# Kernel optimization log

Measured on AMD Instinct MI355X. Metric: run time of the kernel, lower is better.

## Reference

```python
import jax, jax.numpy as jnp
import numpy as np

N = 4096          # nodes (single graph, batch=None)
E = 65536         # edges (avg degree 16)
C = 256           # hidden_channels
L = 3             # num_layers
H = 8             # attention heads
EPS = 1e-5        # batchnorm eps


def setup_inputs() -> dict:
    key = jax.random.key(0)
    ks = iter(jax.random.split(key, 64))
    s = 0.05
    d = {}
    d['x'] = jax.random.normal(next(ks), (N, 1), dtype=jnp.float32)
    d['edge_index'] = jax.random.randint(next(ks), (2, E), 0, N, dtype=jnp.int32)
    # input projection Linear(1, C)
    d['lin1_w'] = jax.random.normal(next(ks), (C, 1), dtype=jnp.float32) * s
    d['lin1_b'] = jnp.zeros((C,), dtype=jnp.float32)
    # GIN MLP: Linear(C,C) -> ReLU -> Linear(C,C), stacked over layers
    d['gin_w1'] = jax.random.normal(next(ks), (L, C, C), dtype=jnp.float32) * s
    d['gin_b1'] = jnp.zeros((L, C), dtype=jnp.float32)
    d['gin_w2'] = jax.random.normal(next(ks), (L, C, C), dtype=jnp.float32) * s
    d['gin_b2'] = jnp.zeros((L, C), dtype=jnp.float32)
    # MultiheadAttention projections
    for nm in ['attn_wq', 'attn_wk', 'attn_wv', 'attn_wo']:
        d[nm] = jax.random.normal(next(ks), (L, C, C), dtype=jnp.float32) * s
    for nm in ['attn_bq', 'attn_bk', 'attn_bv', 'attn_bo']:
        d[nm] = jnp.zeros((L, C), dtype=jnp.float32)
    # three BatchNorms per GPSConv layer
    for nm in ['bn1', 'bn2', 'bn3']:
        d[nm + '_g'] = jnp.ones((L, C), dtype=jnp.float32)
        d[nm + '_b'] = jnp.zeros((L, C), dtype=jnp.float32)
    # GPSConv feedforward: Linear(C, 2C) -> ReLU -> Linear(2C, C)
    d['mlp_w1'] = jax.random.normal(next(ks), (L, 2 * C, C), dtype=jnp.float32) * s
    d['mlp_b1'] = jnp.zeros((L, 2 * C), dtype=jnp.float32)
    d['mlp_w2'] = jax.random.normal(next(ks), (L, C, 2 * C), dtype=jnp.float32) * s
    d['mlp_b2'] = jnp.zeros((L, C), dtype=jnp.float32)
    return d


def _bn(v, g, b):
    # training-mode BatchNorm1d over the node dimension (biased variance)
    m = v.mean(0)
    var = v.var(0)
    return (v - m) * jax.lax.rsqrt(var + EPS) * g + b


def _gps_forward(x, edge_index, lin1_w, lin1_b, gin_w1, gin_b1, gin_w2, gin_b2,
                 attn_wq, attn_bq, attn_wk, attn_bk, attn_wv, attn_bv,
                 attn_wo, attn_bo, bn1_g, bn1_b, bn2_g, bn2_b, bn3_g, bn3_b,
                 mlp_w1, mlp_b1, mlp_w2, mlp_b2):
    h = x @ lin1_w.T + lin1_b                     # [N, C]
    src, dst = edge_index[0], edge_index[1]
    dh = C // H
    scale = 1.0 / jnp.sqrt(jnp.float32(dh))
    for l in range(L):
        xin = h
        # --- GIN branch: gather -> scatter-sum -> MLP ---
        agg = jax.ops.segment_sum(xin[src], dst, num_segments=N)   # [N, C]
        z = xin + agg                                               # eps=0
        z = jax.nn.relu(z @ gin_w1[l].T + gin_b1[l]) @ gin_w2[l].T + gin_b2[l]
        h1 = _bn(z + xin, bn1_g[l], bn1_b[l])
        # --- global multihead attention over all N nodes ---
        q = (xin @ attn_wq[l].T + attn_bq[l]).reshape(N, H, dh)
        k = (xin @ attn_wk[l].T + attn_bk[l]).reshape(N, H, dh)
        v = (xin @ attn_wv[l].T + attn_bv[l]).reshape(N, H, dh)
        scores = jnp.einsum('nhd,mhd->hnm', q, k) * scale           # [H, N, N]
        a = jax.nn.softmax(scores, axis=-1)
        o = jnp.einsum('hnm,mhd->nhd', a, v).reshape(N, C)
        o = o @ attn_wo[l].T + attn_bo[l]
        h2 = _bn(o + xin, bn2_g[l], bn2_b[l])
        # --- combine + feedforward ---
        s = h1 + h2
        m = jax.nn.relu(s @ mlp_w1[l].T + mlp_b1[l]) @ mlp_w2[l].T + mlp_b2[l]
        h = _bn(s + m, bn3_g[l], bn3_b[l])
    return h


def reference(x, edge_index, lin1_w, lin1_b, gin_w1, gin_b1, gin_w2, gin_b2,
              attn_wq, attn_bq, attn_wk, attn_bk, attn_wv, attn_bv,
              attn_wo, attn_bo, bn1_g, bn1_b, bn2_g, bn2_b, bn3_g, bn3_b,
              mlp_w1, mlp_b1, mlp_w2, mlp_b2):
    return _gps_forward(x, edge_index, lin1_w, lin1_b, gin_w1, gin_b1, gin_w2,
                        gin_b2, attn_wq, attn_bq, attn_wk, attn_bk, attn_wv,
                        attn_bv, attn_wo, attn_bo, bn1_g, bn1_b, bn2_g, bn2_b,
                        bn3_g, bn3_b, mlp_w1, mlp_b1, mlp_w2, mlp_b2)
```

## Files before the change

kernel.cpp:

```cpp
#include <hip/hip_runtime.h>

#define NN 4096
#define NE 65536
#define C 256
#define NL 3
#define NH 8
#define DH 32
#define EPS 1e-5f
#define SPLIT 2
#define KT8 (NN/128/SPLIT)
#define SR 512

typedef __bf16 bf16x8 __attribute__((ext_vector_type(8)));
typedef __bf16 bf16x4v __attribute__((ext_vector_type(4)));
typedef float f32x4 __attribute__((ext_vector_type(4)));
typedef short bf16x4s __attribute__((ext_vector_type(4)));

#define QSCALE (0.17677669529663687f * 1.4426950408889634f)

#define CC1 (C*C)
#define GS 72

__global__ __launch_bounds__(256) void prep_w(const float* __restrict__ s0,
        const float* __restrict__ s1, const float* __restrict__ s2,
        const float* __restrict__ s3, const float* __restrict__ s4,
        const float* __restrict__ s5, const float* __restrict__ s6,
        const float* __restrict__ s7, __bf16* __restrict__ dst) {
    int g = blockIdx.y;
    int i = (blockIdx.x*256 + threadIdx.x)*4;
    const float* src; int n;
    switch (g) {
        case 0: src=s0; n=3*CC1; break;
        case 1: src=s1; n=3*CC1; break;
        case 2: src=s2; n=3*CC1; break;
        case 3: src=s3; n=3*CC1; break;
        case 4: src=s4; n=3*CC1; break;
        case 5: src=s5; n=3*CC1; break;
        case 6: src=s6; n=6*CC1; break;
        default: src=s7; n=6*CC1; break;
    }
    if (i >= n) return;
    size_t off;
    if (g >= 2 && g <= 4) {
        int l = i >> 16, rem = i & (CC1-1);
        off = (size_t)(6 + 3*l + (g-2))*CC1 + rem;
    } else {
        size_t base = (g==0) ? 0 : (g==1) ? 3*(size_t)CC1 : (g==5) ? 15*(size_t)CC1
                    : (g==6) ? 18*(size_t)CC1 : 24*(size_t)CC1;
        off = base + i;
    }
    float4 t = *(const float4*)(src + i);
    bf16x4v o = {(__bf16)t.x, (__bf16)t.y, (__bf16)t.z, (__bf16)t.w};
    *(bf16x4v*)(dst + off) = o;
}

__global__ __launch_bounds__(256) void lin1_kernel(const float* __restrict__ x,
        const float* __restrict__ w, const float* __restrict__ b,
        __bf16* __restrict__ out) {
    int n = blockIdx.x, c = threadIdx.x;
    out[(size_t)n*C + c] = (__bf16)(x[n]*w[c] + b[c]);
}

__global__ __launch_bounds__(256) void hist_kernel(const int* __restrict__ ei,
        int* __restrict__ cnt) {
    int e = blockIdx.x*256 + threadIdx.x;
    atomicAdd(&cnt[ei[NE + e]], 1);
}

__global__ __launch_bounds__(256) void scan_kernel(const int* __restrict__ cnt,
        int* __restrict__ rowptr, int* __restrict__ cursor) {
    __shared__ int tot[256];
    __shared__ int pre[257];
    int t = threadIdx.x;
    int base = t*16;
    int local[16];
    int s = 0;
    #pragma unroll
    for (int i = 0; i < 16; i++) { local[i] = s; s += cnt[base+i]; }
    tot[t] = s;
    __syncthreads();
    if (t == 0) {
        int acc = 0;
        for (int i = 0; i < 256; i++) { pre[i] = acc; acc += tot[i]; }
        pre[256] = acc;
    }
    __syncthreads();
    int off = pre[t];
    #pragma unroll
    for (int i = 0; i < 16; i++) {
        rowptr[base+i] = off + local[i];
        cursor[base+i] = off + local[i];
    }
    if (t == 0) rowptr[NN] = pre[256];
}

__global__ __launch_bounds__(256) void fill_kernel(const int* __restrict__ ei,
        int* __restrict__ cursor, int* __restrict__ eidsrc) {
    int e = blockIdx.x*256 + threadIdx.x;
    int dst = ei[NE + e], src = ei[e];
    int pos = atomicAdd(&cursor[dst], 1);
    eidsrc[pos] = src;
}

template<int QKV, int BN, int COMB>
__device__ __forceinline__ void gemm_core(int bm, int bn,
        const __bf16* A, const float* A2f, const __bf16* A2b, const __bf16* W,
        const float* b0, const float* b1, const float* b2,
        const __bf16* add1, const __bf16* add2,
        __bf16* out, __bf16* vt, float* stats,
        const float* coefs,
        const float* st1, const float* g1, const float* bb1,
        const float* st2, const float* g2, const float* bb2,
        const float* lsum,
        int K, int Nout, int relu, __bf16* As, __bf16* Ws) {
    int tid = threadIdx.x;
    int wave = tid >> 6, lane = tid & 63;
    int ln = lane & 15, quad = lane >> 4;
    int row = tid >> 2, kseg = (tid & 3) * 16;
    f32x4 acc[4] = {};
    for (int k0 = 0; k0 < K; k0 += 64) {
        __syncthreads();
        {
            bf16x8 a0, a1;
            if constexpr (COMB) {
                int rowg = bm + row;
                int head = (k0 + kseg) >> 5;
                float w[SPLIT];
                float tot = 0.f;
                #pragma unroll
                for (int zz = 0; zz < SPLIT; zz++) {
                    w[zz] = lsum[((size_t)zz*NH + head)*NN + rowg];
                    tot += w[zz];
                }
                float inv = 1.0f / tot;
                float v[16] = {};
                #pragma unroll
                for (int zz = 0; zz < SPLIT; zz++) {
                    const __bf16* p = &A[((size_t)zz*NN + rowg)*C + k0 + kseg];
                    bf16x8 x0 = *(const bf16x8*)p, x1 = *(const bf16x8*)(p + 8);
                    #pragma unroll
                    for (int j = 0; j < 8; j++) {
                        v[j]   += w[zz]*(float)x0[j];
                        v[8+j] += w[zz]*(float)x1[j];
                    }
                }
                #pragma unroll
                for (int j = 0; j < 8; j++) {
                    a0[j] = (__bf16)(v[j]*inv);
                    a1[j] = (__bf16)(v[8+j]*inv);
                }
            } else {
                const __bf16* ap = &A[(size_t)(bm+row)*K + k0 + kseg];
                a0 = *(const bf16x8*)ap;
                a1 = *(const bf16x8*)(ap + 8);
                if constexpr (BN == 1) {
                    const __bf16* p = &A2b[(size_t)(bm+row)*K + k0 + kseg];
                    bf16x8 z0 = *(const bf16x8*)p;
                    bf16x8 z1v = *(const bf16x8*)(p + 8);
                    float sc1[16], sh1[16], sc2[16], sh2[16];
                    #pragma unroll
                    for (int i = 0; i < 4; i++) {
                        *(float4*)&sc1[i*4] = *(const float4*)&coefs[k0 + kseg + i*4];
                        *(float4*)&sh1[i*4] = *(const float4*)&coefs[C + k0 + kseg + i*4];
                        *(float4*)&sc2[i*4] = *(const float4*)&coefs[2*C + k0 + kseg + i*4];
                        *(float4*)&sh2[i*4] = *(const float4*)&coefs[3*C + k0 + kseg + i*4];
                    }
                    #pragma unroll
                    for (int j = 0; j < 8; j++) {
                        a0[j] = (__bf16)((float)a0[j]*sc1[j] + sh1[j]
                                       + (float)z0[j]*sc2[j] + sh2[j]);
                        a1[j] = (__bf16)((float)a1[j]*sc1[8+j] + sh1[8+j]
                                       + (float)z1v[j]*sc2[8+j] + sh2[8+j]);
                    }
                } else if (A2f) {
                    const float* p = &A2f[(size_t)(bm+row)*K + k0 + kseg];
                    float4 t0 = *(const float4*)p;
                    float4 t1 = *(const float4*)(p+4);
                    float4 t2 = *(const float4*)(p+8);
                    float4 t3 = *(const float4*)(p+12);
                    a0[0]=(__bf16)((float)a0[0]+t0.x); a0[1]=(__bf16)((float)a0[1]+t0.y);
                    a0[2]=(__bf16)((float)a0[2]+t0.z); a0[3]=(__bf16)((float)a0[3]+t0.w);
                    a0[4]=(__bf16)((float)a0[4]+t1.x); a0[5]=(__bf16)((float)a0[5]+t1.y);
                    a0[6]=(__bf16)((float)a0[6]+t1.z); a0[7]=(__bf16)((float)a0[7]+t1.w);
                    a1[0]=(__bf16)((float)a1[0]+t2.x); a1[1]=(__bf16)((float)a1[1]+t2.y);
                    a1[2]=(__bf16)((float)a1[2]+t2.z); a1[3]=(__bf16)((float)a1[3]+t2.w);
                    a1[4]=(__bf16)((float)a1[4]+t3.x); a1[5]=(__bf16)((float)a1[5]+t3.y);
                    a1[6]=(__bf16)((float)a1[6]+t3.z); a1[7]=(__bf16)((float)a1[7]+t3.w);
                }
            }
            *(bf16x8*)&As[row*GS + kseg]     = a0;
            *(bf16x8*)&As[row*GS + kseg + 8] = a1;
            const __bf16* wp = &W[(size_t)(bn+row)*K + k0 + kseg];
            *(bf16x8*)&Ws[row*GS + kseg]     = *(const bf16x8*)wp;
            *(bf16x8*)&Ws[row*GS + kseg + 8] = *(const bf16x8*)(wp + 8);
        }
        __syncthreads();
        #pragma unroll
        for (int kt2 = 0; kt2 < 2; kt2++) {
            bf16x8 bfr = *(const bf16x8*)&Ws[(wave*16+ln)*GS + kt2*32 + quad*8];
            #pragma unroll
            for (int i = 0; i < 4; i++) {
                bf16x8 afr = *(const bf16x8*)&As[(i*16+ln)*GS + kt2*32 + quad*8];
                acc[i] = __builtin_amdgcn_mfma_f32_16x16x32_bf16(afr, bfr, acc[i], 0, 0, 0);
            }
        }
    }
    int col = bn + wave*16 + ln;
    if constexpr (QKV) {
        float bsv = col < 256 ? b0[col] : (col < 512 ? b1[col-256] : b2[col-512]);
        if (col < 512) {
            float osc = col < 256 ? (float)QSCALE : 1.0f;
            #pragma unroll
            for (int i = 0; i < 4; i++)
                #pragma unroll
                for (int rr = 0; rr < 4; rr++)
                    out[(size_t)(bm + i*16 + quad*4 + rr)*SR + col] =
                        (__bf16)((acc[i][rr] + bsv) * osc);
        } else {
            int vrow = col - 512;
            #pragma unroll
            for (int i = 0; i < 4; i++) {
                bf16x4v pk = {(__bf16)(acc[i][0]+bsv), (__bf16)(acc[i][1]+bsv),
                              (__bf16)(acc[i][2]+bsv), (__bf16)(acc[i][3]+bsv)};
                *(bf16x4v*)&vt[(size_t)vrow*NN + bm + i*16 + quad*4] = pk;
            }
        }
        return;
    }
    float bsv = b0[col];
    float sc1 = 0.f, sh1 = 0.f, sc2 = 0.f, sh2 = 0.f;
    if constexpr (BN == 2) {
        float m1 = st1[col]*(1.f/NN);
        sc1 = rsqrtf(st1[C+col]*(1.f/NN) - m1*m1 + EPS) * g1[col];
        sh1 = bb1[col] - m1*sc1;
        float m2 = st2[col]*(1.f/NN);
        sc2 = rsqrtf(st2[C+col]*(1.f/NN) - m2*m2 + EPS) * g2[col];
        sh2 = bb2[col] - m2*sc2;
    }
    float ssum = 0.f, ssq = 0.f;
    #pragma unroll
    for (int i = 0; i < 4; i++) {
        #pragma unroll
        for (int rr = 0; rr < 4; rr++) {
            int rw = bm + i*16 + quad*4 + rr;
            float vv = acc[i][rr] + bsv;
            if (relu) vv = fmaxf(vv, 0.f);
            size_t idx = (size_t)rw*Nout + col;
            if constexpr (BN == 2) {
                vv += (float)add1[idx]*sc1 + sh1 + (float)add2[idx]*sc2 + sh2;
            } else {
                if (add1) vv += (float)add1[idx];
                if (add2) vv += (float)add2[idx];
            }
            out[idx] = (__bf16)vv;
            ssum += vv; ssq += vv*vv;
        }
    }
    if (stats) {
        ssum += __shfl_xor(ssum, 16); ssum += __shfl_xor(ssum, 32);
        ssq  += __shfl_xor(ssq, 16);  ssq  += __shfl_xor(ssq, 32);
        if (quad == 0) {
            atomicAdd(&stats[col], ssum);
            atomicAdd(&stats[Nout + col], ssq);
        }
    }
}

__device__ __forceinline__ void attn_body(int t, const __bf16* __restrict__ qk,
        const __bf16* __restrict__ vt, __bf16* __restrict__ opart,
        float* __restrict__ lsum, __bf16* lds) {
    int z = t >> 8, head = (t >> 5) & 7, qb = (t & 31) * 128;
    int hb = head * DH;
    int tid = threadIdx.x;
    int wave = tid >> 6, lane = tid & 63;
    int ln = lane & 15, quad = lane >> 4;
    __bf16* Kb0 = lds;
    __bf16* Kb1 = lds + 4608;

    bf16x8 qf[2];
    #pragma unroll
    for (int g = 0; g < 2; g++)
        qf[g] = *(const bf16x8*)&qk[(size_t)(qb + wave*32 + g*16 + ln)*SR + hb + quad*8];

    f32x4 ot[2][2] = {};
    float l_[2] = {0.f, 0.f};

    int srow = tid >> 1, sseg = (tid & 1) * 16;
    int kt0 = z * KT8;
    {
        const __bf16* kp = &qk[(size_t)(kt0*128 + srow)*SR + 256 + hb + sseg];
        *(bf16x8*)&Kb0[srow*36 + sseg]     = *(const bf16x8*)kp;
        *(bf16x8*)&Kb0[srow*36 + sseg + 8] = *(const bf16x8*)(kp + 8);
    }
    const __bf16* vbase = &vt[(size_t)(hb + ln)*NN + quad*4];
    const size_t vh = (size_t)16*NN;
    for (int i = 0; i < KT8; i++) {
        int kb = (kt0 + i) * 128;
        __bf16* Kc = (i & 1) ? Kb1 : Kb0;
        __bf16* Kn = (i & 1) ? Kb0 : Kb1;
        __syncthreads();
        bf16x8 nk0, nk1;
        bool hasNext = (i + 1 < KT8);
        if (hasNext) {
            const __bf16* kp = &qk[(size_t)(kb + 128 + srow)*SR + 256 + hb + sseg];
            nk0 = *(const bf16x8*)kp;
            nk1 = *(const bf16x8*)(kp + 8);
        }
        bf16x4s vfc[2][2], vfn[2][2];
        #pragma unroll
        for (int s = 0; s < 2; s++)
            #pragma unroll
            for (int h = 0; h < 2; h++)
                vfc[s][h] = *(const bf16x4s*)&vbase[vh*h + kb + s*16];
        #pragma unroll
        for (int pr = 0; pr < 4; pr++) {
            if (pr < 3) {
                #pragma unroll
                for (int s = 0; s < 2; s++)
                    #pragma unroll
                    for (int h = 0; h < 2; h++)
                        vfn[s][h] = *(const bf16x4s*)&vbase[vh*h + kb + (pr*2+2+s)*16];
            }
            bf16x8 kf0 = *(const bf16x8*)&Kc[((pr*2+0)*16+ln)*36 + quad*8];
            bf16x8 kf1 = *(const bf16x8*)&Kc[((pr*2+1)*16+ln)*36 + quad*8];
            f32x4 zz = {0.f,0.f,0.f,0.f};
            f32x4 st00 = __builtin_amdgcn_mfma_f32_16x16x32_bf16(kf0, qf[0], zz, 0, 0, 0);
            f32x4 st10 = __builtin_amdgcn_mfma_f32_16x16x32_bf16(kf0, qf[1], zz, 0, 0, 0);
            f32x4 st01 = __builtin_amdgcn_mfma_f32_16x16x32_bf16(kf1, qf[0], zz, 0, 0, 0);
            f32x4 st11 = __builtin_amdgcn_mfma_f32_16x16x32_bf16(kf1, qf[1], zz, 0, 0, 0);
            union { __bf16 b[4]; bf16x4s s; } pf00, pf01, pf10, pf11;
            #pragma unroll
            for (int rr = 0; rr < 4; rr++) {
                float p;
                p = __builtin_amdgcn_exp2f(st00[rr]); pf00.b[rr] = (__bf16)p; l_[0] += p;
                p = __builtin_amdgcn_exp2f(st01[rr]); pf01.b[rr] = (__bf16)p; l_[0] += p;
                p = __builtin_amdgcn_exp2f(st10[rr]); pf10.b[rr] = (__bf16)p; l_[1] += p;
                p = __builtin_amdgcn_exp2f(st11[rr]); pf11.b[rr] = (__bf16)p; l_[1] += p;
            }
            ot[0][0] = __builtin_amdgcn_mfma_f32_16x16x16bf16_1k(vfc[0][0], pf00.s, ot[0][0], 0, 0, 0);
            ot[0][1] = __builtin_amdgcn_mfma_f32_16x16x16bf16_1k(vfc[0][1], pf00.s, ot[0][1], 0, 0, 0);
            ot[1][0] = __builtin_amdgcn_mfma_f32_16x16x16bf16_1k(vfc[0][0], pf10.s, ot[1][0], 0, 0, 0);
            ot[1][1] = __builtin_amdgcn_mfma_f32_16x16x16bf16_1k(vfc[0][1], pf10.s, ot[1][1], 0, 0, 0);
            ot[0][0] = __builtin_amdgcn_mfma_f32_16x16x16bf16_1k(vfc[1][0], pf01.s, ot[0][0], 0, 0, 0);
            ot[0][1] = __builtin_amdgcn_mfma_f32_16x16x16bf16_1k(vfc[1][1], pf01.s, ot[0][1], 0, 0, 0);
            ot[1][0] = __builtin_amdgcn_mfma_f32_16x16x16bf16_1k(vfc[1][0], pf11.s, ot[1][0], 0, 0, 0);
            ot[1][1] = __builtin_amdgcn_mfma_f32_16x16x16bf16_1k(vfc[1][1], pf11.s, ot[1][1], 0, 0, 0);
            #pragma unroll
            for (int s = 0; s < 2; s++)
                #pragma unroll
                for (int h = 0; h < 2; h++)
                    vfc[s][h] = vfn[s][h];
        }
        if (hasNext) {
            *(bf16x8*)&Kn[srow*36 + sseg]     = nk0;
            *(bf16x8*)&Kn[srow*36 + sseg + 8] = nk1;
        }
    }
    #pragma unroll
    for (int g = 0; g < 2; g++) {
        l_[g] += __shfl_xor(l_[g], 16);
        l_[g] += __shfl_xor(l_[g], 32);
        float inv = 1.0f / l_[g];
        int qrow = qb + wave*32 + g*16 + ln;
        #pragma unroll
        for (int h = 0; h < 2; h++) {
            bf16x4v pk = {(__bf16)(ot[g][h][0]*inv), (__bf16)(ot[g][h][1]*inv),
                          (__bf16)(ot[g][h][2]*inv), (__bf16)(ot[g][h][3]*inv)};
            *(bf16x4v*)&opart[((size_t)z*NN + qrow)*C + hb + h*16 + quad*4] = pk;
        }
        if (quad == 0)
            lsum[((size_t)z*NH + head)*NN + qrow] = l_[g];
    }
}

__global__ __launch_bounds__(256) void qkv_agg_kernel(const __bf16* __restrict__ Hb,
        const __bf16* __restrict__ Wqkv, const float* __restrict__ bq,
        const float* __restrict__ bk, const float* __restrict__ bv,
        __bf16* __restrict__ qkout, __bf16* __restrict__ vtout,
        const int* __restrict__ rowptr, const int* __restrict__ eidsrc,
        float* __restrict__ agg) {
    __shared__ __bf16 lds[9216];
    int bx = blockIdx.x;
    if (bx < 768) {
        gemm_core<1,0,0>((bx & 63)*64, (bx >> 6)*64, Hb, nullptr, nullptr, Wqkv,
                bq, bk, bv, nullptr, nullptr, qkout, vtout, nullptr,
                nullptr, nullptr, nullptr, nullptr, nullptr, nullptr, nullptr,
                nullptr, C, 768, 0, lds, lds + 4608);
        return;
    }
    int tid = threadIdx.x;
    int wave = tid >> 6, lane = tid & 63;
    int node = (bx - 768)*4 + wave;
    int beg = rowptr[node], end = rowptr[node+1];
    float s0 = 0.f, s1 = 0.f, s2 = 0.f, s3 = 0.f;
    for (int e = beg; e < end; e++) {
        int src = eidsrc[e];
        bf16x4v hv = *(const bf16x4v*)&Hb[(size_t)src*C + lane*4];
        s0 += (float)hv[0]; s1 += (float)hv[1];
        s2 += (float)hv[2]; s3 += (float)hv[3];
    }
    float4 o = {s0, s1, s2, s3};
    *(float4*)&agg[(size_t)node*C + lane*4] = o;
}

__global__ __launch_bounds__(256) void gin1_attn_kernel(const __bf16* __restrict__ Hb,
        const float* __restrict__ agg, const __bf16* __restrict__ gw1,
        const float* __restrict__ gb1, __bf16* __restrict__ t1,
        const __bf16* __restrict__ qk, const __bf16* __restrict__ vt,
        __bf16* __restrict__ opart, float* __restrict__ lsum) {
    __shared__ __bf16 lds[9216];
    int bx = blockIdx.x;
    if (bx < 32*NH*SPLIT) {
        attn_body(bx, qk, vt, opart, lsum, lds);
        return;
    }
    int g = bx - 32*NH*SPLIT;
    gemm_core<0,0,0>((g >> 2)*64, (g & 3)*64, Hb, agg, nullptr, gw1,
            gb1, nullptr, nullptr, nullptr, nullptr, t1, nullptr, nullptr,
            nullptr, nullptr, nullptr, nullptr, nullptr, nullptr, nullptr,
            nullptr, C, C, 1, lds, lds + 4608);
}

__global__ __launch_bounds__(256) void gin2_proj_kernel(const __bf16* __restrict__ t1,
        const __bf16* __restrict__ gw2, const float* __restrict__ gb2,
        const __bf16* __restrict__ Hb, __bf16* __restrict__ z1, float* __restrict__ st1,
        const __bf16* __restrict__ opart, const float* __restrict__ lsum,
        const __bf16* __restrict__ wop, const float* __restrict__ lbo,
        __bf16* __restrict__ z2, float* __restrict__ st2) {
    __shared__ __bf16 lds[9216];
    int bx = blockIdx.x;
    if (bx < 256) {
        gemm_core<0,0,0>((bx >> 2)*64, (bx & 3)*64, t1, nullptr, nullptr, gw2,
                gb2, nullptr, nullptr, Hb, nullptr, z1, nullptr, st1,
                nullptr, nullptr, nullptr, nullptr, nullptr, nullptr, nullptr,
                nullptr, C, C, 0, lds, lds + 4608);
        return;
    }
    int t = bx - 256;
    gemm_core<0,0,1>((t >> 2)*64, (t & 3)*64, opart, nullptr, nullptr, wop,
            lbo, nullptr, nullptr, Hb, nullptr, z2, nullptr, st2,
            nullptr, nullptr, nullptr, nullptr, nullptr, nullptr, nullptr,
            lsum, C, C, 0, lds, lds + 4608);
}

__global__ __launch_bounds__(256) void ff1_kernel(const __bf16* __restrict__ z1,
        const __bf16* __restrict__ z2, const __bf16* __restrict__ mw1,
        const float* __restrict__ lmb1, __bf16* __restrict__ hidden,
        const float* __restrict__ st1, const float* __restrict__ g1,
        const float* __restrict__ bb1, const float* __restrict__ st2,
        const float* __restrict__ g2, const float* __restrict__ bb2) {
    __shared__ __bf16 lds[9216];
    __shared__ float coefs[4*C];
    int tid = threadIdx.x;
    {
        float m = st1[tid]*(1.f/NN);
        float var = st1[C+tid]*(1.f/NN) - m*m;
        float s = rsqrtf(var + EPS) * g1[tid];
        coefs[tid] = s; coefs[C+tid] = bb1[tid] - m*s;
        m = st2[tid]*(1.f/NN);
        var = st2[C+tid]*(1.f/NN) - m*m;
        s = rsqrtf(var + EPS) * g2[tid];
        coefs[2*C+tid] = s; coefs[3*C+tid] = bb2[tid] - m*s;
    }
    int bx = blockIdx.x;
    gemm_core<0,1,0>((bx >> 3)*64, (bx & 7)*64, z1, nullptr, z2, mw1,
            lmb1, nullptr, nullptr, nullptr, nullptr, hidden, nullptr, nullptr,
            coefs, nullptr, nullptr, nullptr, nullptr, nullptr, nullptr,
            nullptr, C, 2*C, 1, lds, lds + 4608);
}

__global__ __launch_bounds__(256) void ff2_kernel(const __bf16* __restrict__ hidden,
        const __bf16* __restrict__ mw2, const float* __restrict__ lmb2,
        const __bf16* __restrict__ z1, const __bf16* __restrict__ z2,
        __bf16* __restrict__ zbuf3, float* __restrict__ st3,
        const float* __restrict__ st1, const float* __restrict__ g1,
        const float* __restrict__ bb1, const float* __restrict__ st2,
        const float* __restrict__ g2, const float* __restrict__ bb2) {
    __shared__ __bf16 lds[9216];
    int bx = blockIdx.x;
    gemm_core<0,2,0>((bx >> 2)*64, (bx & 3)*64, hidden, nullptr, nullptr, mw2,
            lmb2, nullptr, nullptr, z1, z2, zbuf3, nullptr, st3,
            nullptr, st1, g1, bb1, st2, g2, bb2,
            nullptr, 2*C, C, 0, lds, lds + 4608);
}

__global__ __launch_bounds__(256) void bn_apply_kernel(const __bf16* __restrict__ z,
        const float* __restrict__ stats, const float* __restrict__ g,
        const float* __restrict__ b, __bf16* __restrict__ outb,
        float* __restrict__ outf) {
    int idx4 = (blockIdx.x*256 + threadIdx.x) * 4;
    int c = idx4 & (C-1);
    bf16x4v zv = *(const bf16x4v*)&z[idx4];
    float4 st = *(const float4*)&stats[c];
    float4 sq = *(const float4*)&stats[C + c];
    float4 gv = *(const float4*)&g[c];
    float4 bv = *(const float4*)&b[c];
    float o[4];
    float m0 = st.x*(1.f/NN), m1 = st.y*(1.f/NN), m2 = st.z*(1.f/NN), m3 = st.w*(1.f/NN);
    o[0] = ((float)zv[0] - m0) * rsqrtf(sq.x*(1.f/NN) - m0*m0 + EPS) * gv.x + bv.x;
    o[1] = ((float)zv[1] - m1) * rsqrtf(sq.y*(1.f/NN) - m1*m1 + EPS) * gv.y + bv.y;
    o[2] = ((float)zv[2] - m2) * rsqrtf(sq.z*(1.f/NN) - m2*m2 + EPS) * gv.z + bv.z;
    o[3] = ((float)zv[3] - m3) * rsqrtf(sq.w*(1.f/NN) - m3*m3 + EPS) * gv.w + bv.w;
    if (outb) {
        bf16x4v ov = {(__bf16)o[0], (__bf16)o[1], (__bf16)o[2], (__bf16)o[3]};
        *(bf16x4v*)&outb[idx4] = ov;
    } else {
        float4 ov = {o[0], o[1], o[2], o[3]};
        *(float4*)&outf[idx4] = ov;
    }
}

extern "C" void kernel_launch(void* const* d_in, const int* in_sizes, int n_in,
                              void* d_out, int out_size, void* d_ws, size_t ws_size,
                              hipStream_t stream) {
    const float* x      = (const float*)d_in[0];
    const int*   ei     = (const int*)d_in[1];
    const float* lin1_w = (const float*)d_in[2];
    const float* lin1_b = (const float*)d_in[3];
    const float* gin_w1 = (const float*)d_in[4];
    const float* gin_b1 = (const float*)d_in[5];
    const float* gin_w2 = (const float*)d_in[6];
    const float* gin_b2 = (const float*)d_in[7];
    const float* wq = (const float*)d_in[8];
    const float* wk = (const float*)d_in[9];
    const float* wv = (const float*)d_in[10];
    const float* wo = (const float*)d_in[11];
    const float* bq = (const float*)d_in[12];
    const float* bk = (const float*)d_in[13];
    const float* bv = (const float*)d_in[14];
    const float* bo = (const float*)d_in[15];
    const float* bn1_g = (const float*)d_in[16];
    const float* bn1_b = (const float*)d_in[17];
    const float* bn2_g = (const float*)d_in[18];
    const float* bn2_b = (const float*)d_in[19];
    const float* bn3_g = (const float*)d_in[20];
    const float* bn3_b = (const float*)d_in[21];
    const float* mw1 = (const float*)d_in[22];
    const float* mb1 = (const float*)d_in[23];
    const float* mw2 = (const float*)d_in[24];
    const float* mb2 = (const float*)d_in[25];

    const size_t MB = 1u << 20;
    char* ws = (char*)d_ws;
    __bf16* Hb      = (__bf16*)(ws);
    __bf16* z1      = (__bf16*)(ws + 2*MB);
    __bf16* zbuf3   = (__bf16*)(ws + 4*MB);
    __bf16* z2      = (__bf16*)(ws + 6*MB);
    __bf16* t1      = (__bf16*)(ws + 8*MB);
    __bf16* QKbuf   = (__bf16*)(ws + 10*MB);
    __bf16* Vt      = (__bf16*)(ws + 14*MB);
    float*  agg     = (float*)(ws + 16*MB);
    __bf16* Opart   = (__bf16*)(ws + 20*MB);
    __bf16* hiddenb = (__bf16*)(ws + 24*MB);
    __bf16* Wb      = (__bf16*)(ws + 28*MB);
    float*  stats   = (float*)(ws + 32*MB);
    int*    cursor  = (int*)(ws + 32*MB + 64*1024);
    int*    rowptr  = (int*)(ws + 32*MB + 96*1024);
    int*    eidsrc  = (int*)(ws + 32*MB + 128*1024);
    float*  lsum    = (float*)(ws + 33*MB);

    dim3 blk(256);

    prep_w<<<dim3(384, 8), blk, 0, stream>>>(gin_w1, gin_w2, wq, wk, wv, wo, mw1, mw2, Wb);
    hipMemsetAsync(stats, 0, 9 * 2 * C * sizeof(float), stream);
    lin1_kernel<<<NN, blk, 0, stream>>>(x, lin1_w, lin1_b, Hb);
    hipMemsetAsync(cursor, 0, NN * sizeof(int), stream);
    hist_kernel<<<NE/256, blk, 0, stream>>>(ei, cursor);
    scan_kernel<<<1, blk, 0, stream>>>(cursor, rowptr, cursor);
    fill_kernel<<<NE/256, blk, 0, stream>>>(ei, cursor, eidsrc);

    for (int l = 0; l < NL; l++) {
        const __bf16* gw1b = Wb + (size_t)l*CC1;
        const __bf16* gw2b = Wb + (size_t)(3+l)*CC1;
        const __bf16* wqkv = Wb + (size_t)(6+3*l)*CC1;
        const __bf16* wop  = Wb + (size_t)(15+l)*CC1;
        const __bf16* mw1p = Wb + (size_t)(18+2*l)*CC1;
        const __bf16* mw2p = Wb + (size_t)(24+2*l)*CC1;
        const float* gb1 = gin_b1 + (size_t)l*C;
        const float* gb2 = gin_b2 + (size_t)l*C;
        const float* lbq = bq + (size_t)l*C;
        const float* lbk = bk + (size_t)l*C;
        const float* lbv = bv + (size_t)l*C;
        const float* lbo = bo + (size_t)l*C;
        const float* lmb1 = mb1 + (size_t)l*2*C;
        const float* lmb2 = mb2 + (size_t)l*C;
        float* st1 = stats + (size_t)l*3*2*C;
        float* st2 = st1 + 2*C;
        float* st3 = st2 + 2*C;
        const float* g1v = bn1_g + (size_t)l*C; const float* b1v = bn1_b + (size_t)l*C;
        const float* g2v = bn2_g + (size_t)l*C; const float* b2v = bn2_b + (size_t)l*C;

        qkv_agg_kernel<<<768 + NN/4, blk, 0, stream>>>(Hb, wqkv, lbq, lbk, lbv,
                QKbuf, Vt, rowptr, eidsrc, agg);
        gin1_attn_kernel<<<32*NH*SPLIT + 256, blk, 0, stream>>>(Hb, agg,
                gw1b, gb1, t1, QKbuf, Vt, Opart, lsum);
        gin2_proj_kernel<<<512, blk, 0, stream>>>(t1, gw2b, gb2, Hb, z1, st1,
                Opart, lsum, wop, lbo, z2, st2);
        ff1_kernel<<<512, blk, 0, stream>>>(z1, z2, mw1p, lmb1, hiddenb,
                st1, g1v, b1v, st2, g2v, b2v);
        ff2_kernel<<<256, blk, 0, stream>>>(hiddenb, mw2p, lmb2, z1, z2,
                zbuf3, st3, st1, g1v, b1v, st2, g2v, b2v);
        if (l == NL-1)
            bn_apply_kernel<<<NN/4, blk, 0, stream>>>(zbuf3, st3,
                    bn3_g + (size_t)l*C, bn3_b + (size_t)l*C, nullptr, (float*)d_out);
        else
            bn_apply_kernel<<<NN/4, blk, 0, stream>>>(zbuf3, st3,
                    bn3_g + (size_t)l*C, bn3_b + (size_t)l*C, Hb, nullptr);
    }
}
```

Measured before the change: 474.5 us.

## Halve attention query tile per block and compute row sums with MFMA

Each attention block now handles 64 query rows instead of 128, with one 16-row group per wave, which doubles the attention grid for more parallelism across CUs. The softmax denominator is now accumulated by an extra MFMA against a vector of ones instead of scalar adds followed by cross-lane shuffles. This cuts VALU work and register pressure, but each K tile staged in LDS and each V fragment is now reused by half as many queries, so total K/V traffic doubles. The row sums are also taken from bf16-rounded probabilities, which slightly changes numerics.

Result: slower. 653.7 us (+37.8%).

```diff
diff --git a/kernel.cpp b/kernel.cpp
--- a/kernel.cpp
+++ b/kernel.cpp
@@ -10,6 +10,7 @@
 #define SPLIT 2
 #define KT8 (NN/128/SPLIT)
 #define SR 512
+#define ATTN_BLKS ((NN/64)*NH*SPLIT)
 
 typedef __bf16 bf16x8 __attribute__((ext_vector_type(8)));
 typedef __bf16 bf16x4v __attribute__((ext_vector_type(4)));
@@ -269,7 +270,7 @@
 __device__ __forceinline__ void attn_body(int t, const __bf16* __restrict__ qk,
         const __bf16* __restrict__ vt, __bf16* __restrict__ opart,
         float* __restrict__ lsum, __bf16* lds) {
-    int z = t >> 8, head = (t >> 5) & 7, qb = (t & 31) * 128;
+    int z = t >> 9, head = (t >> 6) & 7, qb = (t & 63) * 64;
     int hb = head * DH;
     int tid = threadIdx.x;
     int wave = tid >> 6, lane = tid & 63;
@@ -277,13 +278,11 @@
     __bf16* Kb0 = lds;
     __bf16* Kb1 = lds + 4608;
 
-    bf16x8 qf[2];
-    #pragma unroll
-    for (int g = 0; g < 2; g++)
-        qf[g] = *(const bf16x8*)&qk[(size_t)(qb + wave*32 + g*16 + ln)*SR + hb + quad*8];
-
-    f32x4 ot[2][2] = {};
-    float l_[2] = {0.f, 0.f};
+    bf16x8 qf = *(const bf16x8*)&qk[(size_t)(qb + wave*16 + ln)*SR + hb + quad*8];
+
+    f32x4 ot[2] = {};
+    f32x4 lacc = {};
+    const bf16x4s ones = {(short)0x3F80, (short)0x3F80, (short)0x3F80, (short)0x3F80};
 
     int srow = tid >> 1, sseg = (tid & 1) * 16;
     int kt0 = z * KT8;
@@ -324,27 +323,20 @@
             bf16x8 kf0 = *(const bf16x8*)&Kc[((pr*2+0)*16+ln)*36 + quad*8];
             bf16x8 kf1 = *(const bf16x8*)&Kc[((pr*2+1)*16+ln)*36 + quad*8];
             f32x4 zz = {0.f,0.f,0.f,0.f};
-            f32x4 st00 = __builtin_amdgcn_mfma_f32_16x16x32_bf16(kf0, qf[0], zz, 0, 0, 0);
-            f32x4 st10 = __builtin_amdgcn_mfma_f32_16x16x32_bf16(kf0, qf[1], zz, 0, 0, 0);
-            f32x4 st01 = __builtin_amdgcn_mfma_f32_16x16x32_bf16(kf1, qf[0], zz, 0, 0, 0);
-            f32x4 st11 = __builtin_amdgcn_mfma_f32_16x16x32_bf16(kf1, qf[1], zz, 0, 0, 0);
-            union { __bf16 b[4]; bf16x4s s; } pf00, pf01, pf10, pf11;
+            f32x4 st0 = __builtin_amdgcn_mfma_f32_16x16x32_bf16(kf0, qf, zz, 0, 0, 0);
+            f32x4 st1 = __builtin_amdgcn_mfma_f32_16x16x32_bf16(kf1, qf, zz, 0, 0, 0);
+            union { __bf16 b[4]; bf16x4s s; } pf0, pf1;
             #pragma unroll
             for (int rr = 0; rr < 4; rr++) {
-                float p;
-                p = __builtin_amdgcn_exp2f(st00[rr]); pf00.b[rr] = (__bf16)p; l_[0] += p;
-                p = __builtin_amdgcn_exp2f(st01[rr]); pf01.b[rr] = (__bf16)p; l_[0] += p;
-                p = __builtin_amdgcn_exp2f(st10[rr]); pf10.b[rr] = (__bf16)p; l_[1] += p;
-                p = __builtin_amdgcn_exp2f(st11[rr]); pf11.b[rr] = (__bf16)p; l_[1] += p;
+                pf0.b[rr] = (__bf16)__builtin_amdgcn_exp2f(st0[rr]);
+                pf1.b[rr] = (__bf16)__builtin_amdgcn_exp2f(st1[rr]);
             }
-            ot[0][0] = __builtin_amdgcn_mfma_f32_16x16x16bf16_1k(vfc[0][0], pf00.s, ot[0][0], 0, 0, 0);
-            ot[0][1] = __builtin_amdgcn_mfma_f32_16x16x16bf16_1k(vfc[0][1], pf00.s, ot[0][1], 0, 0, 0);
-            ot[1][0] = __builtin_amdgcn_mfma_f32_16x16x16bf16_1k(vfc[0][0], pf10.s, ot[1][0], 0, 0, 0);
-            ot[1][1] = __builtin_amdgcn_mfma_f32_16x16x16bf16_1k(vfc[0][1], pf10.s, ot[1][1], 0, 0, 0);
-            ot[0][0] = __builtin_amdgcn_mfma_f32_16x16x16bf16_1k(vfc[1][0], pf01.s, ot[0][0], 0, 0, 0);
-            ot[0][1] = __builtin_amdgcn_mfma_f32_16x16x16bf16_1k(vfc[1][1], pf01.s, ot[0][1], 0, 0, 0);
-            ot[1][0] = __builtin_amdgcn_mfma_f32_16x16x16bf16_1k(vfc[1][0], pf11.s, ot[1][0], 0, 0, 0);
-            ot[1][1] = __builtin_amdgcn_mfma_f32_16x16x16bf16_1k(vfc[1][1], pf11.s, ot[1][1], 0, 0, 0);
+            ot[0] = __builtin_amdgcn_mfma_f32_16x16x16bf16_1k(vfc[0][0], pf0.s, ot[0], 0, 0, 0);
+            ot[1] = __builtin_amdgcn_mfma_f32_16x16x16bf16_1k(vfc[0][1], pf0.s, ot[1], 0, 0, 0);
+            lacc  = __builtin_amdgcn_mfma_f32_16x16x16bf16_1k(ones,      pf0.s, lacc,  0, 0, 0);
+            ot[0] = __builtin_amdgcn_mfma_f32_16x16x16bf16_1k(vfc[1][0], pf1.s, ot[0], 0, 0, 0);
+            ot[1] = __builtin_amdgcn_mfma_f32_16x16x16bf16_1k(vfc[1][1], pf1.s, ot[1], 0, 0, 0);
+            lacc  = __builtin_amdgcn_mfma_f32_16x16x16bf16_1k(ones,      pf1.s, lacc,  0, 0, 0);
             #pragma unroll
             for (int s = 0; s < 2; s++)
                 #pragma unroll
@@ -356,21 +348,17 @@
             *(bf16x8*)&Kn[srow*36 + sseg + 8] = nk1;
         }
     }
+    float l_ = lacc[0];
+    float inv = 1.0f / l_;
+    int qrow = qb + wave*16 + ln;
     #pragma unroll
-    for (int g = 0; g < 2; g++) {
-        l_[g] += __shfl_xor(l_[g], 16);
-        l_[g] += __shfl_xor(l_[g], 32);
-        float inv = 1.0f / l_[g];
-        int qrow = qb + wave*32 + g*16 + ln;
-        #pragma unroll
-        for (int h = 0; h < 2; h++) {
-            bf16x4v pk = {(__bf16)(ot[g][h][0]*inv), (__bf16)(ot[g][h][1]*inv),
-                          (__bf16)(ot[g][h][2]*inv), (__bf16)(ot[g][h][3]*inv)};
-            *(bf16x4v*)&opart[((size_t)z*NN + qrow)*C + hb + h*16 + quad*4] = pk;
-        }
-        if (quad == 0)
-            lsum[((size_t)z*NH + head)*NN + qrow] = l_[g];
-    }
+    for (int h = 0; h < 2; h++) {
+        bf16x4v pk = {(__bf16)(ot[h][0]*inv), (__bf16)(ot[h][1]*inv),
+                      (__bf16)(ot[h][2]*inv), (__bf16)(ot[h][3]*inv)};
+        *(bf16x4v*)&opart[((size_t)z*NN + qrow)*C + hb + h*16 + quad*4] = pk;
+    }
+    if (quad == 0)
+        lsum[((size_t)z*NH + head)*NN + qrow] = l_;
 }
 
 __global__ __launch_bounds__(256) void qkv_agg_kernel(const __bf16* __restrict__ Hb,
@@ -410,11 +398,11 @@
         __bf16* __restrict__ opart, float* __restrict__ lsum) {
     __shared__ __bf16 lds[9216];
     int bx = blockIdx.x;
-    if (bx < 32*NH*SPLIT) {
+    if (bx < ATTN_BLKS) {
         attn_body(bx, qk, vt, opart, lsum, lds);
         return;
     }
-    int g = bx - 32*NH*SPLIT;
+    int g = bx - ATTN_BLKS;
     gemm_core<0,0,0>((g >> 2)*64, (g & 3)*64, Hb, agg, nullptr, gw1,
             gb1, nullptr, nullptr, nullptr, nullptr, t1, nullptr, nullptr,
             nullptr, nullptr, nullptr, nullptr, nullptr, nullptr, nullptr,
@@ -592,7 +580,7 @@
 
         qkv_agg_kernel<<<768 + NN/4, blk, 0, stream>>>(Hb, wqkv, lbq, lbk, lbv,
                 QKbuf, Vt, rowptr, eidsrc, agg);
-        gin1_attn_kernel<<<32*NH*SPLIT + 256, blk, 0, stream>>>(Hb, agg,
+        gin1_attn_kernel<<<ATTN_BLKS + 256, blk, 0, stream>>>(Hb, agg,
                 gw1b, gb1, t1, QKbuf, Vt, Opart, lsum);
         gin2_proj_kernel<<<512, blk, 0, stream>>>(t1, gw2b, gb2, Hb, z1, st1,
                 Opart, lsum, wop, lbo, z2, st2);
```

## Stage V tiles through LDS and compute softmax row sums with MFMA

Applied to the files above, without the earlier changes.

The attention body now double-buffers the V^T tile in shared memory alongside K, so V fragments come from LDS instead of scattered global loads issued per iteration. The softmax denominator is accumulated with extra MFMAs against a ones vector, replacing per-element scalar adds and the final cross-lane shuffles. This raises LDS per block from about 18KB to about 35KB, which can reduce occupancy. It also adds MFMA work, and the sum is now taken over bf16-rounded probabilities.

New measurement: 423.9 us. 10.6% less time.

```diff
diff --git a/kernel.cpp b/kernel.cpp
--- a/kernel.cpp
+++ b/kernel.cpp
@@ -10,6 +10,8 @@
 #define SPLIT 2
 #define KT8 (NN/128/SPLIT)
 #define SR 512
+#define ATTN_BLKS ((NN/128)*NH*SPLIT)
+#define VS 136
 
 typedef __bf16 bf16x8 __attribute__((ext_vector_type(8)));
 typedef __bf16 bf16x4v __attribute__((ext_vector_type(4)));
@@ -276,6 +278,8 @@
     int ln = lane & 15, quad = lane >> 4;
     __bf16* Kb0 = lds;
     __bf16* Kb1 = lds + 4608;
+    __bf16* Vb0 = lds + 9216;
+    __bf16* Vb1 = lds + 9216 + 32*VS;
 
     bf16x8 qf[2];
     #pragma unroll
@@ -283,46 +287,47 @@
         qf[g] = *(const bf16x8*)&qk[(size_t)(qb + wave*32 + g*16 + ln)*SR + hb + quad*8];
 
     f32x4 ot[2][2] = {};
-    float l_[2] = {0.f, 0.f};
+    f32x4 la[2] = {};
+    const bf16x4s ones = {(short)0x3F80, (short)0x3F80, (short)0x3F80, (short)0x3F80};
 
     int srow = tid >> 1, sseg = (tid & 1) * 16;
+    int vd = tid >> 3, vseg = (tid & 7) * 16;
     int kt0 = z * KT8;
     {
         const __bf16* kp = &qk[(size_t)(kt0*128 + srow)*SR + 256 + hb + sseg];
         *(bf16x8*)&Kb0[srow*36 + sseg]     = *(const bf16x8*)kp;
         *(bf16x8*)&Kb0[srow*36 + sseg + 8] = *(const bf16x8*)(kp + 8);
-    }
-    const __bf16* vbase = &vt[(size_t)(hb + ln)*NN + quad*4];
-    const size_t vh = (size_t)16*NN;
+        const __bf16* vp = &vt[(size_t)(hb + vd)*NN + kt0*128 + vseg];
+        *(bf16x8*)&Vb0[vd*VS + vseg]     = *(const bf16x8*)vp;
+        *(bf16x8*)&Vb0[vd*VS + vseg + 8] = *(const bf16x8*)(vp + 8);
+    }
     for (int i = 0; i < KT8; i++) {
         int kb = (kt0 + i) * 128;
         __bf16* Kc = (i & 1) ? Kb1 : Kb0;
         __bf16* Kn = (i & 1) ? Kb0 : Kb1;
+        __bf16* Vc = (i & 1) ? Vb1 : Vb0;
+        __bf16* Vn = (i & 1) ? Vb0 : Vb1;
         __syncthreads();
-        bf16x8 nk0, nk1;
+        bf16x8 nk0, nk1, nv0, nv1;
         bool hasNext = (i + 1 < KT8);
         if (hasNext) {
             const __bf16* kp = &qk[(size_t)(kb + 128 + srow)*SR + 256 + hb + sseg];
             nk0 = *(const bf16x8*)kp;
             nk1 = *(const bf16x8*)(kp + 8);
-        }
-        bf16x4s vfc[2][2], vfn[2][2];
-        #pragma unroll
-        for (int s = 0; s < 2; s++)
-            #pragma unroll
-            for (int h = 0; h < 2; h++)
-                vfc[s][h] = *(const bf16x4s*)&vbase[vh*h + kb + s*16];
+            const __bf16* vp = &vt[(size_t)(hb + vd)*NN + kb + 128 + vseg];
+            nv0 = *(const bf16x8*)vp;
+            nv1 = *(const bf16x8*)(vp + 8);
+        }
         #pragma unroll
         for (int pr = 0; pr < 4; pr++) {
-            if (pr < 3) {
-                #pragma unroll
-                for (int s = 0; s < 2; s++)
-                    #pragma unroll
-                    for (int h = 0; h < 2; h++)
-                        vfn[s][h] = *(const bf16x4s*)&vbase[vh*h + kb + (pr*2+2+s)*16];
-            }
             bf16x8 kf0 = *(const bf16x8*)&Kc[((pr*2+0)*16+ln)*36 + quad*8];
             bf16x8 kf1 = *(const bf16x8*)&Kc[((pr*2+1)*16+ln)*36 + quad*8];
+            bf16x4s vf[2][2];
+            #pragma unroll
+            for (int s = 0; s < 2; s++)
+                #pragma unroll
+                for (int h = 0; h < 2; h++)
+                    vf[s][h] = *(const bf16x4s*)&Vc[(h*16+ln)*VS + (pr*2+s)*16 + quad*4];
             f32x4 zz = {0.f,0.f,0.f,0.f};
             f32x4 st00 = __builtin_amdgcn_mfma_f32_16x16x32_bf16(kf0, qf[0], zz, 0, 0, 0);
             f32x4 st10 = __builtin_amdgcn_mfma_f32_16x16x32_bf16(kf0, qf[1], zz, 0, 0, 0);
@@ -331,36 +336,35 @@
             union { __bf16 b[4]; bf16x4s s; } pf00, pf01, pf10, pf11;
             #pragma unroll
             for (int rr = 0; rr < 4; rr++) {
-                float p;
-                p = __builtin_amdgcn_exp2f(st00[rr]); pf00.b[rr] = (__bf16)p; l_[0] += p;
-                p = __builtin_amdgcn_exp2f(st01[rr]); pf01.b[rr] = (__bf16)p; l_[0] += p;
-                p = __builtin_amdgcn_exp2f(st10[rr]); pf10.b[rr] = (__bf16)p; l_[1] += p;
-                p = __builtin_amdgcn_exp2f(st11[rr]); pf11.b[rr] = (__bf16)p; l_[1] += p;
+                pf00.b[rr] = (__bf16)__builtin_amdgcn_exp2f(st00[rr]);
+                pf01.b[rr] = (__bf16)__builtin_amdgcn_exp2f(st01[rr]);
+                pf10.b[rr] = (__bf16)__builtin_amdgcn_exp2f(st10[rr]);
+                pf11.b[rr] = (__bf16)__builtin_amdgcn_exp2f(st11[rr]);
             }
-            ot[0][0] = __builtin_amdgcn_mfma_f32_16x16x16bf16_1k(vfc[0][0], pf00.s, ot[0][0], 0, 0, 0);
-            ot[0][1] = __builtin_amdgcn_mfma_f32_16x16x16bf16_1k(vfc[0][1], pf00.s, ot[0][1], 0, 0, 0);
-            ot[1][0] = __builtin_amdgcn_mfma_f32_16x16x16bf16_1k(vfc[0][0], pf10.s, ot[1][0], 0, 0, 0);
-            ot[1][1] = __builtin_amdgcn_mfma_f32_16x16x16bf16_1k(vfc[0][1], pf10.s, ot[1][1], 0, 0, 0);
-            ot[0][0] = __builtin_amdgcn_mfma_f32_16x16x16bf16_1k(vfc[1][0], pf01.s, ot[0][0], 0, 0, 0);
-            ot[0][1] = __builtin_amdgcn_mfma_f32_16x16x16bf16_1k(vfc[1][1], pf01.s, ot[0][1], 0, 0, 0);
-            ot[1][0] = __builtin_amdgcn_mfma_f32_16x16x16bf16_1k(vfc[1][0], pf11.s, ot[1][0], 0, 0, 0);
-            ot[1][1] = __builtin_amdgcn_mfma_f32_16x16x16bf16_1k(vfc[1][1], pf11.s, ot[1][1], 0, 0, 0);
-            #pragma unroll
-            for (int s = 0; s < 2; s++)
-                #pragma unroll
-                for (int h = 0; h < 2; h++)
-                    vfc[s][h] = vfn[s][h];
+            ot[0][0] = __builtin_amdgcn_mfma_f32_16x16x16bf16_1k(vf[0][0], pf00.s, ot[0][0], 0, 0, 0);
+            ot[0][1] = __builtin_amdgcn_mfma_f32_16x16x16bf16_1k(vf[0][1], pf00.s, ot[0][1], 0, 0, 0);
+            ot[1][0] = __builtin_amdgcn_mfma_f32_16x16x16bf16_1k(vf[0][0], pf10.s, ot[1][0], 0, 0, 0);
+            ot[1][1] = __builtin_amdgcn_mfma_f32_16x16x16bf16_1k(vf[0][1], pf10.s, ot[1][1], 0, 0, 0);
+            la[0]    = __builtin_amdgcn_mfma_f32_16x16x16bf16_1k(ones,     pf00.s, la[0],    0, 0, 0);
+            la[1]    = __builtin_amdgcn_mfma_f32_16x16x16bf16_1k(ones,     pf10.s, la[1],    0, 0, 0);
+            ot[0][0] = __builtin_amdgcn_mfma_f32_16x16x16bf16_1k(vf[1][0], pf01.s, ot[0][0], 0, 0, 0);
+            ot[0][1] = __builtin_amdgcn_mfma_f32_16x16x16bf16_1k(vf[1][1], pf01.s, ot[0][1], 0, 0, 0);
+            ot[1][0] = __builtin_amdgcn_mfma_f32_16x16x16bf16_1k(vf[1][0], pf11.s, ot[1][0], 0, 0, 0);
+            ot[1][1] = __builtin_amdgcn_mfma_f32_16x16x16bf16_1k(vf[1][1], pf11.s, ot[1][1], 0, 0, 0);
+            la[0]    = __builtin_amdgcn_mfma_f32_16x16x16bf16_1k(ones,     pf01.s, la[0],    0, 0, 0);
+            la[1]    = __builtin_amdgcn_mfma_f32_16x16x16bf16_1k(ones,     pf11.s, la[1],    0, 0, 0);
         }
         if (hasNext) {
             *(bf16x8*)&Kn[srow*36 + sseg]     = nk0;
             *(bf16x8*)&Kn[srow*36 + sseg + 8] = nk1;
+            *(bf16x8*)&Vn[vd*VS + vseg]     = nv0;
+            *(bf16x8*)&Vn[vd*VS + vseg + 8] = nv1;
         }
     }
     #pragma unroll
     for (int g = 0; g < 2; g++) {
-        l_[g] += __shfl_xor(l_[g], 16);
-        l_[g] += __shfl_xor(l_[g], 32);
-        float inv = 1.0f / l_[g];
+        float l_ = la[g][0];
+        float inv = 1.0f / l_;
         int qrow = qb + wave*32 + g*16 + ln;
         #pragma unroll
         for (int h = 0; h < 2; h++) {
@@ -369,7 +373,7 @@
             *(bf16x4v*)&opart[((size_t)z*NN + qrow)*C + hb + h*16 + quad*4] = pk;
         }
         if (quad == 0)
-            lsum[((size_t)z*NH + head)*NN + qrow] = l_[g];
+            lsum[((size_t)z*NH + head)*NN + qrow] = l_;
     }
 }
 
@@ -408,13 +412,13 @@
         const float* __restrict__ gb1, __bf16* __restrict__ t1,
         const __bf16* __restrict__ qk, const __bf16* __restrict__ vt,
         __bf16* __restrict__ opart, float* __restrict__ lsum) {
-    __shared__ __bf16 lds[9216];
+    __shared__ __bf16 lds[17920];
     int bx = blockIdx.x;
-    if (bx < 32*NH*SPLIT) {
+    if (bx < ATTN_BLKS) {
         attn_body(bx, qk, vt, opart, lsum, lds);
         return;
     }
-    int g = bx - 32*NH*SPLIT;
+    int g = bx - ATTN_BLKS;
     gemm_core<0,0,0>((g >> 2)*64, (g & 3)*64, Hb, agg, nullptr, gw1,
             gb1, nullptr, nullptr, nullptr, nullptr, t1, nullptr, nullptr,
             nullptr, nullptr, nullptr, nullptr, nullptr, nullptr, nullptr,
@@ -592,7 +596,7 @@
 
         qkv_agg_kernel<<<768 + NN/4, blk, 0, stream>>>(Hb, wqkv, lbq, lbk, lbv,
                 QKbuf, Vt, rowptr, eidsrc, agg);
-        gin1_attn_kernel<<<32*NH*SPLIT + 256, blk, 0, stream>>>(Hb, agg,
+        gin1_attn_kernel<<<ATTN_BLKS + 256, blk, 0, stream>>>(Hb, agg,
                 gw1b, gb1, t1, QKbuf, Vt, Opart, lsum);
         gin2_proj_kernel<<<512, blk, 0, stream>>>(t1, gw2b, gb2, Hb, z1, st1,
                 Opart, lsum, wop, lbo, z2, st2);
```
